# Performance work log

Hardware: AMD Instinct MI355X
Metric: run time of the kernel (lower is better)

## Reference

```python
import jax, jax.numpy as jnp
import numpy as np

B, IN_CH, SLOTS, SLOT_SIZE, READ_SLOTS = 16, 512, 10000, 256, 3


def _fa_params(key, c, scale=0.02):
    k1, k2 = jax.random.split(key)
    return (jax.random.normal(k1, (c, c), jnp.float32) * scale, jnp.zeros((c,), jnp.float32),
            jax.random.normal(k2, (c, c), jnp.float32) * scale, jnp.zeros((c,), jnp.float32))


def fast_attention(x, w1, b1, w2, b2):
    # FastAttention: x * Linear2(softmax(Linear1(x), dim=channel))
    h = jax.nn.softmax(x @ w1 + b1, axis=1)
    return x * (h @ w2 + b2)


def setup_inputs() -> dict:
    key = jax.random.key(0)
    ks = jax.random.split(key, 12)
    s = 0.02
    inp = {}
    inp["inputs"] = jax.random.normal(ks[0], (B, IN_CH), jnp.float32)
    inp["memory"] = jax.random.normal(ks[1], (B, SLOTS, SLOT_SIZE), jnp.float32)
    # read_weights branch: FastAttention(IN_CH) -> Linear(IN_CH, READ_SLOTS*SLOTS) -> tanh
    inp["fa_r_w1"], inp["fa_r_b1"], inp["fa_r_w2"], inp["fa_r_b2"] = _fa_params(ks[2], IN_CH)
    inp["W_read"] = jax.random.normal(ks[3], (IN_CH, READ_SLOTS * SLOTS), jnp.float32) * s
    inp["b_read"] = jnp.zeros((READ_SLOTS * SLOTS,), jnp.float32)
    # update_weights branch: FastAttention(IN_CH) -> Linear(IN_CH, READ_SLOTS) -> sigmoid
    inp["fa_u_w1"], inp["fa_u_b1"], inp["fa_u_w2"], inp["fa_u_b2"] = _fa_params(ks[4], IN_CH)
    inp["W_uw"] = jax.random.normal(ks[5], (IN_CH, READ_SLOTS), jnp.float32) * s
    inp["b_uw"] = jnp.zeros((READ_SLOTS,), jnp.float32)
    # update_memory branch: FastAttention(IN_CH+SLOT_SIZE) -> Linear(., SLOT_SIZE) -> relu
    inp["fa_um_w1"], inp["fa_um_b1"], inp["fa_um_w2"], inp["fa_um_b2"] = _fa_params(ks[6], IN_CH + SLOT_SIZE)
    inp["W_um"] = jax.random.normal(ks[7], (IN_CH + SLOT_SIZE, SLOT_SIZE), jnp.float32) * s
    inp["b_um"] = jnp.zeros((SLOT_SIZE,), jnp.float32)
    # apply_memory branch: FastAttention(2*SLOT_SIZE) -> Linear(., SLOT_SIZE) -> relu
    inp["fa_am_w1"], inp["fa_am_b1"], inp["fa_am_w2"], inp["fa_am_b2"] = _fa_params(ks[8], 2 * SLOT_SIZE)
    inp["W_am"] = jax.random.normal(ks[9], (2 * SLOT_SIZE, SLOT_SIZE), jnp.float32) * s
    inp["b_am"] = jnp.zeros((SLOT_SIZE,), jnp.float32)
    return inp


def reference(inputs, memory,
              fa_r_w1, fa_r_b1, fa_r_w2, fa_r_b2, W_read, b_read,
              fa_u_w1, fa_u_b1, fa_u_w2, fa_u_b2, W_uw, b_uw,
              fa_um_w1, fa_um_b1, fa_um_w2, fa_um_b2, W_um, b_um,
              fa_am_w1, fa_am_b1, fa_am_w2, fa_am_b2, W_am, b_am):
    b = inputs.shape[0]
    # read scores: [B, READ_SLOTS, SLOTS]
    read = jnp.tanh(fast_attention(inputs, fa_r_w1, fa_r_b1, fa_r_w2, fa_r_b2) @ W_read + b_read)
    read = read.reshape(b, READ_SLOTS, SLOTS)
    read_w = jnp.max(read, axis=2)                 # [B, READ_SLOTS]
    read_idx = jnp.argmax(read, axis=2)            # [B, READ_SLOTS] int
    upd_w = jax.nn.sigmoid(fast_attention(inputs, fa_u_w1, fa_u_b1, fa_u_w2, fa_u_b2) @ W_uw + b_uw)
    # gather the selected memory slots: [B, READ_SLOTS, SLOT_SIZE]
    r_all = memory[jnp.arange(b)[:, None], read_idx]
    m = jnp.zeros((b, SLOT_SIZE), inputs.dtype)
    # sequential recurrence over the (small, fixed) read_slots
    for i in range(READ_SLOTS):
        r = r_all[:, i]                            # [B, SLOT_SIZE]
        upd = jax.nn.relu(fast_attention(jnp.concatenate([r, inputs], axis=1),
                                         fa_um_w1, fa_um_b1, fa_um_w2, fa_um_b2) @ W_um + b_um)
        u = upd_w[:, i:i + 1]
        r = u * upd + (1.0 - u) * r
        m = read_w[:, i:i + 1] * jax.nn.relu(fast_attention(jnp.concatenate([r, m], axis=1),
                                                            fa_am_w1, fa_am_b1, fa_am_w2, fa_am_b2) @ W_am + b_am)
    return jnp.tanh(m)
```

## Files before the change

kernel.cpp:

```cpp
#include <hip/hip_runtime.h>
#include <cfloat>
#include <cmath>

constexpr int NTILES = 79;

enum : int {
  WS_XR    = 0,
  WS_UPDW  = 8192,
  WS_READW = 8240,
  WS_PMAX  = 8288,
  WS_PIDX  = 12080,
  WS_RNEW  = 15872,
  WS_M     = 28160,
  WS_XC    = 32256,
  WS_TPA   = 69120,
  WS_HA    = 134656,
  WS_YPA   = 151040,
  WS_TPU   = 216576,
  WS_HU    = 437760,
  WS_YPU   = 474624,
  WS_WPU   = 695808,
  WS_TPM   = 769536,
  WS_HM    = 802304,
  WS_YPM   = 810496,
  WS_WPM   = 843264,
};

__device__ __forceinline__ float wave_sum(float v) {
#pragma unroll
  for (int o = 32; o > 0; o >>= 1) v += __shfl_xor(v, o);
  return v;
}
__device__ __forceinline__ float wave_max(float v) {
#pragma unroll
  for (int o = 32; o > 0; o >>= 1) v = fmaxf(v, __shfl_xor(v, o));
  return v;
}
__device__ __forceinline__ float block_sum(float v, float* red) {
  int lane = threadIdx.x & 63, w = threadIdx.x >> 6, nw = blockDim.x >> 6;
  v = wave_sum(v);
  __syncthreads();
  if (lane == 0) red[w] = v;
  __syncthreads();
  float s = 0.f;
  for (int k = 0; k < nw; k++) s += red[k];
  return s;
}
__device__ __forceinline__ float block_max(float v, float* red) {
  int lane = threadIdx.x & 63, w = threadIdx.x >> 6, nw = blockDim.x >> 6;
  v = wave_max(v);
  __syncthreads();
  if (lane == 0) red[w] = v;
  __syncthreads();
  float s = -FLT_MAX;
  for (int k = 0; k < nw; k++) s = fmaxf(s, red[k]);
  return s;
}

__device__ __forceinline__ void mm_tile16(
    const float* __restrict__ xs,
    const float* __restrict__ W, int ldw,
    int koff, int jbase, float2& ra, float2& rb) {
  int lane = threadIdx.x & 63, w = threadIdx.x >> 6;
  const float* xa = xs + (w * 2) * 128;
  const float* xb = xa + 128;
  const float* Wp = W + (size_t)koff * ldw + jbase + lane * 2;
  float a00 = 0.f, a01 = 0.f, a10 = 0.f, a11 = 0.f;
#pragma unroll 8
  for (int k = 0; k < 128; k++) {
    float2 wv = *(const float2*)(Wp + (size_t)k * ldw);
    float xav = xa[k], xbv = xb[k];
    a00 = fmaf(xav, wv.x, a00); a01 = fmaf(xav, wv.y, a01);
    a10 = fmaf(xbv, wv.x, a10); a11 = fmaf(xbv, wv.y, a11);
  }
  ra = make_float2(a00, a01);
  rb = make_float2(a10, a11);
}
__device__ __forceinline__ void store_tile16(
    float* __restrict__ T, int ldt, int jbase, float2 ra, float2 rb) {
  int lane = threadIdx.x & 63, w = threadIdx.x >> 6;
  int r0 = w * 2, j0 = jbase + lane * 2;
  *(float2*)(T + (size_t)r0 * ldt + j0) = ra;
  *(float2*)(T + (size_t)(r0 + 1) * ldt + j0) = rb;
}

__global__ __launch_bounds__(512) void k_mm1_a(
    const float* __restrict__ x, const float* __restrict__ w1r,
    const float* __restrict__ w1u, float* __restrict__ TPA) {
  __shared__ float xs[16 * 128];
  int jt = blockIdx.x, ks = blockIdx.y, m = blockIdx.z, tid = threadIdx.x;
  for (int t = tid; t < 2048; t += 512) {
    int b = t >> 7, kk = t & 127;
    xs[t] = x[b * 512 + ks * 128 + kk];
  }
  __syncthreads();
  float2 ra, rb;
  mm_tile16(xs, m ? w1u : w1r, 512, ks * 128, jt * 128, ra, rb);
  store_tile16(TPA + (size_t)((m * 4 + ks) * 16) * 512, 512, jt * 128, ra, rb);
}

__global__ __launch_bounds__(512) void k_sm_a(
    const float* __restrict__ TPA, const float* __restrict__ b1r,
    const float* __restrict__ b1u, float* __restrict__ HA) {
  __shared__ float red[16];
  int b = blockIdx.x, m = blockIdx.y, tid = threadIdx.x;
  float t = (m ? b1u : b1r)[tid];
#pragma unroll
  for (int ks = 0; ks < 4; ks++)
    t += TPA[(size_t)((m * 4 + ks) * 16 + b) * 512 + tid];
  float mx = block_max(t, red);
  float e = expf(t - mx);
  float s = block_sum(e, red);
  HA[(size_t)(m * 16 + b) * 512 + tid] = e / s;
}

__global__ __launch_bounds__(512) void k_mm2_a(
    const float* __restrict__ HA, const float* __restrict__ w2r,
    const float* __restrict__ w2u, float* __restrict__ YPA) {
  __shared__ float xs[16 * 128];
  int jt = blockIdx.x, ks = blockIdx.y, m = blockIdx.z, tid = threadIdx.x;
  for (int t = tid; t < 2048; t += 512) {
    int b = t >> 7, kk = t & 127;
    xs[t] = HA[(size_t)(m * 16 + b) * 512 + ks * 128 + kk];
  }
  __syncthreads();
  float2 ra, rb;
  mm_tile16(xs, m ? w2u : w2r, 512, ks * 128, jt * 128, ra, rb);
  store_tile16(YPA + (size_t)((m * 4 + ks) * 16) * 512, 512, jt * 128, ra, rb);
}

__global__ __launch_bounds__(512) void k_fin_a(
    const float* __restrict__ x, const float* __restrict__ YPA,
    const float* __restrict__ b2r, const float* __restrict__ b2u,
    const float* __restrict__ Wuw, const float* __restrict__ buw,
    float* __restrict__ XR, float* __restrict__ UPDW, float* __restrict__ M) {
  __shared__ float red[16];
  int b = blockIdx.x, tid = threadIdx.x;
  float yr = b2r[tid], yu = b2u[tid];
#pragma unroll
  for (int ks = 0; ks < 4; ks++) {
    yr += YPA[(size_t)((0 + ks) * 16 + b) * 512 + tid];
    yu += YPA[(size_t)((4 + ks) * 16 + b) * 512 + tid];
  }
  float xv = x[b * 512 + tid];
  XR[b * 512 + tid] = xv * yr;
  float xu = xv * yu;
  if (tid < 256) M[b * 256 + tid] = 0.f;
  for (int i = 0; i < 3; i++) {
    float si = block_sum(xu * Wuw[tid * 3 + i], red);
    if (tid == 0) UPDW[b * 3 + i] = 1.f / (1.f + expf(-(si + buw[i])));
  }
}

__global__ __launch_bounds__(512) void k_read(
    const float* __restrict__ W, const float* __restrict__ brd,
    const float* __restrict__ xr,
    float* __restrict__ pmax, int* __restrict__ pidx) {
  __shared__ __align__(16) float xs[16 * 512];
  int tid = threadIdx.x, lane = tid & 63, w = tid >> 6;
  int i = blockIdx.y, tile = blockIdx.x;
  {
    const float4* s4 = (const float4*)xr;
    float4* d4 = (float4*)xs;
    for (int t = tid; t < 2048; t += 512) d4[t] = s4[t];
  }
  __syncthreads();
  int b0 = w * 2, b1 = b0 + 1;
  int s0 = tile * 128 + lane * 2;
  int sC = (s0 > 9998) ? 9998 : s0;
  const float* Wp = W + i * 10000 + sC;
  const float* xap = xs + b0 * 512;
  const float* xbp = xs + b1 * 512;
  float a00 = 0.f, a01 = 0.f, a10 = 0.f, a11 = 0.f;
#pragma unroll 8
  for (int c = 0; c < 512; c += 4) {
    float4 xa = *(const float4*)(xap + c);
    float4 xb = *(const float4*)(xbp + c);
    float2 w0 = *(const float2*)(Wp + (size_t)(c + 0) * 30000);
    float2 w1 = *(const float2*)(Wp + (size_t)(c + 1) * 30000);
    float2 w2 = *(const float2*)(Wp + (size_t)(c + 2) * 30000);
    float2 w3 = *(const float2*)(Wp + (size_t)(c + 3) * 30000);
    a00 = fmaf(xa.x, w0.x, a00); a01 = fmaf(xa.x, w0.y, a01);
    a10 = fmaf(xb.x, w0.x, a10); a11 = fmaf(xb.x, w0.y, a11);
    a00 = fmaf(xa.y, w1.x, a00); a01 = fmaf(xa.y, w1.y, a01);
    a10 = fmaf(xb.y, w1.x, a10); a11 = fmaf(xb.y, w1.y, a11);
    a00 = fmaf(xa.z, w2.x, a00); a01 = fmaf(xa.z, w2.y, a01);
    a10 = fmaf(xb.z, w2.x, a10); a11 = fmaf(xb.z, w2.y, a11);
    a00 = fmaf(xa.w, w3.x, a00); a01 = fmaf(xa.w, w3.y, a01);
    a10 = fmaf(xb.w, w3.x, a10); a11 = fmaf(xb.w, w3.y, a11);
  }
  float2 bb = *(const float2*)(brd + i * 10000 + sC);
  bool ok0 = (s0 < 10000), ok1 = (s0 + 1 < 10000);
  float v00 = a00 + bb.x, v01 = a01 + bb.y;
  float v10 = a10 + bb.x, v11 = a11 + bb.y;
  float bv0 = ok0 ? v00 : -FLT_MAX; int bi0 = s0;
  if (ok1 && v01 > bv0) { bv0 = v01; bi0 = s0 + 1; }
  float bv1 = ok0 ? v10 : -FLT_MAX; int bi1 = s0;
  if (ok1 && v11 > bv1) { bv1 = v11; bi1 = s0 + 1; }
#pragma unroll
  for (int o = 32; o > 0; o >>= 1) {
    float ov = __shfl_down(bv0, o); int oi = __shfl_down(bi0, o);
    if (ov > bv0) { bv0 = ov; bi0 = oi; }
    ov = __shfl_down(bv1, o); oi = __shfl_down(bi1, o);
    if (ov > bv1) { bv1 = ov; bi1 = oi; }
  }
  if (lane == 0) {
    int base = (i * 16 + b0) * NTILES + tile;
    pmax[base] = bv0; pidx[base] = bi0;
    base = (i * 16 + b1) * NTILES + tile;
    pmax[base] = bv1; pidx[base] = bi1;
  }
}

__global__ __launch_bounds__(768) void k_gather(
    const float* __restrict__ mem, const float* __restrict__ x,
    const float* __restrict__ pmax, const int* __restrict__ pidx,
    float* __restrict__ READW, float* __restrict__ XC) {
  __shared__ int sidx;
  int bi = blockIdx.x, b = bi / 3, i = bi % 3;
  int tid = threadIdx.x, lane = tid & 63;
  if (tid < 64) {
    float bv = -FLT_MAX; int bix = 0;
    const float* pm = pmax + (i * 16 + b) * NTILES;
    const int* pi = pidx + (i * 16 + b) * NTILES;
    for (int t = lane; t < NTILES; t += 64) {
      float v = pm[t]; int ix = pi[t];
      if (v > bv || (v == bv && ix < bix)) { bv = v; bix = ix; }
    }
#pragma unroll
    for (int o = 32; o > 0; o >>= 1) {
      float ov = __shfl_down(bv, o); int oi = __shfl_down(bix, o);
      if (ov > bv || (ov == bv && oi < bix)) { bv = ov; bix = oi; }
    }
    if (lane == 0) { sidx = bix; READW[bi] = tanhf(bv); }
  }
  __syncthreads();
  if (tid < 256) XC[(size_t)bi * 768 + tid] = mem[((size_t)b * 10000 + sidx) * 256 + tid];
  else           XC[(size_t)bi * 768 + tid] = x[b * 512 + (tid - 256)];
}

__global__ __launch_bounds__(512) void k_mm1_u(
    const float* __restrict__ XC, const float* __restrict__ w1um,
    float* __restrict__ TPU) {
  __shared__ float xs[16 * 128];
  int jt = blockIdx.x, ks = blockIdx.y, g = blockIdx.z, tid = threadIdx.x;
  for (int t = tid; t < 2048; t += 512) {
    int r = t >> 7, kk = t & 127;
    xs[t] = XC[(size_t)(g * 16 + r) * 768 + ks * 128 + kk];
  }
  __syncthreads();
  float2 ra, rb;
  mm_tile16(xs, w1um, 768, ks * 128, jt * 128, ra, rb);
  store_tile16(TPU + (size_t)(ks * 48 + g * 16) * 768, 768, jt * 128, ra, rb);
}

__global__ __launch_bounds__(768) void k_sm_u(
    const float* __restrict__ TPU, const float* __restrict__ b1um,
    float* __restrict__ HU) {
  __shared__ float red[16];
  int bi = blockIdx.x, tid = threadIdx.x;
  float t = b1um[tid];
#pragma unroll
  for (int ks = 0; ks < 6; ks++)
    t += TPU[(size_t)(ks * 48 + bi) * 768 + tid];
  float mx = block_max(t, red);
  float e = expf(t - mx);
  float s = block_sum(e, red);
  HU[(size_t)bi * 768 + tid] = e / s;
}

__global__ __launch_bounds__(512) void k_mm2_u(
    const float* __restrict__ HU, const float* __restrict__ w2um,
    float* __restrict__ YPU) {
  __shared__ float xs[16 * 128];
  int jt = blockIdx.x, ks = blockIdx.y, g = blockIdx.z, tid = threadIdx.x;
  for (int t = tid; t < 2048; t += 512) {
    int r = t >> 7, kk = t & 127;
    xs[t] = HU[(size_t)(g * 16 + r) * 768 + ks * 128 + kk];
  }
  __syncthreads();
  float2 ra, rb;
  mm_tile16(xs, w2um, 768, ks * 128, jt * 128, ra, rb);
  store_tile16(YPU + (size_t)(ks * 48 + g * 16) * 768, 768, jt * 128, ra, rb);
}

__global__ __launch_bounds__(512) void k_wum(
    const float* __restrict__ YPU, const float* __restrict__ XC,
    const float* __restrict__ b2um, const float* __restrict__ Wum,
    float* __restrict__ WPU) {
  __shared__ float xs[16 * 128];
  int jt = blockIdx.x, ks = blockIdx.y, g = blockIdx.z, tid = threadIdx.x;
  for (int t = tid; t < 2048; t += 512) {
    int r = t >> 7, kk = t & 127;
    int bi = g * 16 + r, k = ks * 128 + kk;
    float y = b2um[k];
#pragma unroll
    for (int k2 = 0; k2 < 6; k2++) y += YPU[(size_t)(k2 * 48 + bi) * 768 + k];
    xs[t] = XC[(size_t)bi * 768 + k] * y;
  }
  __syncthreads();
  float2 ra, rb;
  mm_tile16(xs, Wum, 256, ks * 128, jt * 128, ra, rb);
  store_tile16(WPU + (size_t)(ks * 48 + g * 16) * 256, 256, jt * 128, ra, rb);
}

__global__ __launch_bounds__(256) void k_fin_u(
    const float* __restrict__ WPU, const float* __restrict__ XC,
    const float* __restrict__ bum, const float* __restrict__ UPDW,
    float* __restrict__ RNEW) {
  int bi = blockIdx.x, tid = threadIdx.x;
  float s = bum[tid];
#pragma unroll
  for (int ks = 0; ks < 6; ks++)
    s += WPU[(size_t)(ks * 48 + bi) * 256 + tid];
  float u = UPDW[bi];
  RNEW[(size_t)bi * 256 + tid] = u * fmaxf(s, 0.f) + (1.f - u) * XC[(size_t)bi * 768 + tid];
}

__global__ __launch_bounds__(512) void k_mm1_m(
    const float* __restrict__ RNEW, const float* __restrict__ M,
    const float* __restrict__ w1am, float* __restrict__ TPM, int i) {
  __shared__ float xs[16 * 128];
  int jt = blockIdx.x, ks = blockIdx.y, tid = threadIdx.x;
  for (int t = tid; t < 2048; t += 512) {
    int b = t >> 7, kk = t & 127;
    xs[t] = (ks < 2) ? RNEW[(size_t)(b * 3 + i) * 256 + ks * 128 + kk]
                     : M[b * 256 + (ks - 2) * 128 + kk];
  }
  __syncthreads();
  float2 ra, rb;
  mm_tile16(xs, w1am, 512, ks * 128, jt * 128, ra, rb);
  store_tile16(TPM + (size_t)(ks * 16) * 512, 512, jt * 128, ra, rb);
}

__global__ __launch_bounds__(512) void k_sm_m(
    const float* __restrict__ TPM, const float* __restrict__ b1am,
    float* __restrict__ HM) {
  __shared__ float red[16];
  int b = blockIdx.x, tid = threadIdx.x;
  float t = b1am[tid];
#pragma unroll
  for (int ks = 0; ks < 4; ks++)
    t += TPM[(size_t)(ks * 16 + b) * 512 + tid];
  float mx = block_max(t, red);
  float e = expf(t - mx);
  float s = block_sum(e, red);
  HM[(size_t)b * 512 + tid] = e / s;
}

__global__ __launch_bounds__(512) void k_mm2_m(
    const float* __restrict__ HM, const float* __restrict__ w2am,
    float* __restrict__ YPM) {
  __shared__ float xs[16 * 128];
  int jt = blockIdx.x, ks = blockIdx.y, tid = threadIdx.x;
  for (int t = tid; t < 2048; t += 512) {
    int b = t >> 7, kk = t & 127;
    xs[t] = HM[(size_t)b * 512 + ks * 128 + kk];
  }
  __syncthreads();
  float2 ra, rb;
  mm_tile16(xs, w2am, 512, ks * 128, jt * 128, ra, rb);
  store_tile16(YPM + (size_t)(ks * 16) * 512, 512, jt * 128, ra, rb);
}

__global__ __launch_bounds__(512) void k_wam(
    const float* __restrict__ YPM, const float* __restrict__ RNEW,
    const float* __restrict__ M, const float* __restrict__ b2am,
    const float* __restrict__ Wam, float* __restrict__ WPM, int i) {
  __shared__ float xs[16 * 128];
  int jt = blockIdx.x, ks = blockIdx.y, tid = threadIdx.x;
  for (int t = tid; t < 2048; t += 512) {
    int b = t >> 7, kk = t & 127;
    int k = ks * 128 + kk;
    float xc = (ks < 2) ? RNEW[(size_t)(b * 3 + i) * 256 + k]
                        : M[b * 256 + k - 256];
    float y = b2am[k];
#pragma unroll
    for (int k2 = 0; k2 < 4; k2++) y += YPM[(size_t)(k2 * 16 + b) * 512 + k];
    xs[t] = xc * y;
  }
  __syncthreads();
  float2 ra, rb;
  mm_tile16(xs, Wam, 256, ks * 128, jt * 128, ra, rb);
  store_tile16(WPM + (size_t)(ks * 16) * 256, 256, jt * 128, ra, rb);
}

__global__ __launch_bounds__(256) void k_fin_m(
    const float* __restrict__ WPM, const float* __restrict__ bam,
    const float* __restrict__ READW, float* __restrict__ M,
    float* __restrict__ out, int i, int last) {
  int b = blockIdx.x, tid = threadIdx.x;
  float s = bam[tid];
#pragma unroll
  for (int ks = 0; ks < 4; ks++)
    s += WPM[(size_t)(ks * 16 + b) * 256 + tid];
  float mv = READW[b * 3 + i] * fmaxf(s, 0.f);
  M[b * 256 + tid] = mv;
  if (last) out[b * 256 + tid] = tanhf(mv);
}

extern "C" void kernel_launch(void* const* d_in, const int* in_sizes, int n_in,
                              void* d_out, int out_size, void* d_ws, size_t ws_size,
                              hipStream_t stream) {
  const float* x    = (const float*)d_in[0];
  const float* mem  = (const float*)d_in[1];
  const float* w1r  = (const float*)d_in[2];
  const float* b1r  = (const float*)d_in[3];
  const float* w2r  = (const float*)d_in[4];
  const float* b2r  = (const float*)d_in[5];
  const float* Wrd  = (const float*)d_in[6];
  const float* brd  = (const float*)d_in[7];
  const float* w1u  = (const float*)d_in[8];
  const float* b1u  = (const float*)d_in[9];
  const float* w2u  = (const float*)d_in[10];
  const float* b2u  = (const float*)d_in[11];
  const float* Wuw  = (const float*)d_in[12];
  const float* buw  = (const float*)d_in[13];
  const float* w1um = (const float*)d_in[14];
  const float* b1um = (const float*)d_in[15];
  const float* w2um = (const float*)d_in[16];
  const float* b2um = (const float*)d_in[17];
  const float* Wum  = (const float*)d_in[18];
  const float* bum  = (const float*)d_in[19];
  const float* w1am = (const float*)d_in[20];
  const float* b1am = (const float*)d_in[21];
  const float* w2am = (const float*)d_in[22];
  const float* b2am = (const float*)d_in[23];
  const float* Wam  = (const float*)d_in[24];
  const float* bam  = (const float*)d_in[25];

  float* ws   = (float*)d_ws;
  float* XR   = ws + WS_XR;
  float* UPDW = ws + WS_UPDW;
  float* RDW  = ws + WS_READW;
  float* PMAX = ws + WS_PMAX;
  int*   PIDX = (int*)(ws + WS_PIDX);
  float* RNEW = ws + WS_RNEW;
  float* M    = ws + WS_M;
  float* XC   = ws + WS_XC;
  float* TPA  = ws + WS_TPA;
  float* HA   = ws + WS_HA;
  float* YPA  = ws + WS_YPA;
  float* TPU  = ws + WS_TPU;
  float* HU   = ws + WS_HU;
  float* YPU  = ws + WS_YPU;
  float* WPU  = ws + WS_WPU;
  float* TPM  = ws + WS_TPM;
  float* HM   = ws + WS_HM;
  float* YPM  = ws + WS_YPM;
  float* WPM  = ws + WS_WPM;
  float* out  = (float*)d_out;

  k_mm1_a<<<dim3(4, 4, 2), 512, 0, stream>>>(x, w1r, w1u, TPA);
  k_sm_a <<<dim3(16, 2),   512, 0, stream>>>(TPA, b1r, b1u, HA);
  k_mm2_a<<<dim3(4, 4, 2), 512, 0, stream>>>(HA, w2r, w2u, YPA);
  k_fin_a<<<16,            512, 0, stream>>>(x, YPA, b2r, b2u, Wuw, buw,
                                             XR, UPDW, M);
  k_read  <<<dim3(NTILES, 3), 512, 0, stream>>>(Wrd, brd, XR, PMAX, PIDX);
  k_gather<<<48,              768, 0, stream>>>(mem, x, PMAX, PIDX, RDW, XC);
  k_mm1_u<<<dim3(6, 6, 3), 512, 0, stream>>>(XC, w1um, TPU);
  k_sm_u <<<48,            768, 0, stream>>>(TPU, b1um, HU);
  k_mm2_u<<<dim3(6, 6, 3), 512, 0, stream>>>(HU, w2um, YPU);
  k_wum  <<<dim3(2, 6, 3), 512, 0, stream>>>(YPU, XC, b2um, Wum, WPU);
  k_fin_u<<<48,            256, 0, stream>>>(WPU, XC, bum, UPDW, RNEW);
  for (int i = 0; i < 3; i++) {
    k_mm1_m<<<dim3(4, 4), 512, 0, stream>>>(RNEW, M, w1am, TPM, i);
    k_sm_m <<<16,         512, 0, stream>>>(TPM, b1am, HM);
    k_mm2_m<<<dim3(4, 4), 512, 0, stream>>>(HM, w2am, YPM);
    k_wam  <<<dim3(2, 4), 512, 0, stream>>>(YPM, RNEW, M, b2am, Wam, WPM, i);
    k_fin_m<<<16,         256, 0, stream>>>(WPM, bam, RDW, M, out, i, i == 2);
  }
}
```

Before: 508.1 us.

## Fuse softmax with second matmul and epilogues, dropping split-K partial kernels

Merges each FastAttention softmax with the following Linear2 matmul and the elementwise epilogue into one kernel that keeps the full softmax rows in shared memory. It also folds the update-weight sigmoid into the gather kernel, and folds the final bias/relu/mix steps into the output matmuls. This removes several launches and intermediate global buffers per stage. In exchange, each fused kernel runs the full reduction depth in very few blocks, which reduces parallelism and lengthens per-thread serial loops.

```diff
diff --git a/kernel.cpp b/kernel.cpp
--- a/kernel.cpp
+++ b/kernel.cpp
@@ -12,18 +12,13 @@
   WS_PIDX  = 12080,
   WS_RNEW  = 15872,
   WS_M     = 28160,
-  WS_XC    = 32256,
-  WS_TPA   = 69120,
-  WS_HA    = 134656,
-  WS_YPA   = 151040,
-  WS_TPU   = 216576,
-  WS_HU    = 437760,
-  WS_YPU   = 474624,
-  WS_WPU   = 695808,
-  WS_TPM   = 769536,
-  WS_HM    = 802304,
-  WS_YPM   = 810496,
-  WS_WPM   = 843264,
+  WS_XU    = 32256,
+  WS_XA    = 40448,
+  WS_TPA   = 48640,
+  WS_TPM   = 114176,
+  WS_XU2   = 146944,
+  WS_TPU   = 183808,
+  WS_XC    = 404992,
 };
 
 __device__ __forceinline__ float wave_sum(float v) {
@@ -46,21 +41,11 @@
   for (int k = 0; k < nw; k++) s += red[k];
   return s;
 }
-__device__ __forceinline__ float block_max(float v, float* red) {
-  int lane = threadIdx.x & 63, w = threadIdx.x >> 6, nw = blockDim.x >> 6;
-  v = wave_max(v);
-  __syncthreads();
-  if (lane == 0) red[w] = v;
-  __syncthreads();
-  float s = -FLT_MAX;
-  for (int k = 0; k < nw; k++) s = fmaxf(s, red[k]);
-  return s;
-}
 
 __device__ __forceinline__ void mm_tile16(
     const float* __restrict__ xs,
-    const float* __restrict__ W, int ldw,
-    int koff, int jbase, float2& ra, float2& rb) {
+    const float* __restrict__ W, int ldw, int koff, int jbase,
+    float2& ra, float2& rb) {
   int lane = threadIdx.x & 63, w = threadIdx.x >> 6;
   const float* xa = xs + (w * 2) * 128;
   const float* xb = xa + 128;
@@ -76,12 +61,50 @@
   ra = make_float2(a00, a01);
   rb = make_float2(a10, a11);
 }
+__device__ __forceinline__ void mm_rows(const float* __restrict__ xs, int ldx, int K,
+                                        const float* __restrict__ W, int ldw, int jbase,
+                                        float2& ra, float2& rb) {
+  int lane = threadIdx.x & 63, w = threadIdx.x >> 6;
+  const float* xa = xs + (w * 2) * ldx;
+  const float* xb = xa + ldx;
+  const float* Wp = W + jbase + lane * 2;
+  float a00 = 0.f, a01 = 0.f, a10 = 0.f, a11 = 0.f;
+#pragma unroll 16
+  for (int k = 0; k < K; k++) {
+    float2 wv = *(const float2*)(Wp + (size_t)k * ldw);
+    float xav = xa[k], xbv = xb[k];
+    a00 = fmaf(xav, wv.x, a00); a01 = fmaf(xav, wv.y, a01);
+    a10 = fmaf(xbv, wv.x, a10); a11 = fmaf(xbv, wv.y, a11);
+  }
+  ra = make_float2(a00, a01);
+  rb = make_float2(a10, a11);
+}
 __device__ __forceinline__ void store_tile16(
     float* __restrict__ T, int ldt, int jbase, float2 ra, float2 rb) {
   int lane = threadIdx.x & 63, w = threadIdx.x >> 6;
   int r0 = w * 2, j0 = jbase + lane * 2;
   *(float2*)(T + (size_t)r0 * ldt + j0) = ra;
   *(float2*)(T + (size_t)(r0 + 1) * ldt + j0) = rb;
+}
+
+__device__ __forceinline__ void softmax_rows(float* xs, int ncol) {
+  int lane = threadIdx.x & 63, w = threadIdx.x >> 6;
+#pragma unroll
+  for (int rr = 0; rr < 2; rr++) {
+    float* row = xs + (size_t)(w * 2 + rr) * ncol;
+    float mx = -FLT_MAX;
+    for (int j = lane; j < ncol; j += 64) mx = fmaxf(mx, row[j]);
+    mx = wave_max(mx);
+    float acc = 0.f;
+    for (int j = lane; j < ncol; j += 64) {
+      float e = expf(row[j] - mx);
+      row[j] = e;
+      acc += e;
+    }
+    acc = wave_sum(acc);
+    float inv = 1.f / acc;
+    for (int j = lane; j < ncol; j += 64) row[j] *= inv;
+  }
 }
 
 __global__ __launch_bounds__(512) void k_mm1_a(
@@ -99,57 +122,35 @@
   store_tile16(TPA + (size_t)((m * 4 + ks) * 16) * 512, 512, jt * 128, ra, rb);
 }
 
-__global__ __launch_bounds__(512) void k_sm_a(
-    const float* __restrict__ TPA, const float* __restrict__ b1r,
-    const float* __restrict__ b1u, float* __restrict__ HA) {
-  __shared__ float red[16];
-  int b = blockIdx.x, m = blockIdx.y, tid = threadIdx.x;
-  float t = (m ? b1u : b1r)[tid];
-#pragma unroll
-  for (int ks = 0; ks < 4; ks++)
-    t += TPA[(size_t)((m * 4 + ks) * 16 + b) * 512 + tid];
-  float mx = block_max(t, red);
-  float e = expf(t - mx);
-  float s = block_sum(e, red);
-  HA[(size_t)(m * 16 + b) * 512 + tid] = e / s;
-}
-
-__global__ __launch_bounds__(512) void k_mm2_a(
-    const float* __restrict__ HA, const float* __restrict__ w2r,
-    const float* __restrict__ w2u, float* __restrict__ YPA) {
-  __shared__ float xs[16 * 128];
-  int jt = blockIdx.x, ks = blockIdx.y, m = blockIdx.z, tid = threadIdx.x;
-  for (int t = tid; t < 2048; t += 512) {
-    int b = t >> 7, kk = t & 127;
-    xs[t] = HA[(size_t)(m * 16 + b) * 512 + ks * 128 + kk];
-  }
-  __syncthreads();
-  float2 ra, rb;
-  mm_tile16(xs, m ? w2u : w2r, 512, ks * 128, jt * 128, ra, rb);
-  store_tile16(YPA + (size_t)((m * 4 + ks) * 16) * 512, 512, jt * 128, ra, rb);
-}
-
-__global__ __launch_bounds__(512) void k_fin_a(
-    const float* __restrict__ x, const float* __restrict__ YPA,
+__global__ __launch_bounds__(512) void k_sm2_a(
+    const float* __restrict__ TPA, const float* __restrict__ x,
+    const float* __restrict__ b1r, const float* __restrict__ b1u,
+    const float* __restrict__ w2r, const float* __restrict__ w2u,
     const float* __restrict__ b2r, const float* __restrict__ b2u,
-    const float* __restrict__ Wuw, const float* __restrict__ buw,
-    float* __restrict__ XR, float* __restrict__ UPDW, float* __restrict__ M) {
-  __shared__ float red[16];
-  int b = blockIdx.x, tid = threadIdx.x;
-  float yr = b2r[tid], yu = b2u[tid];
-#pragma unroll
-  for (int ks = 0; ks < 4; ks++) {
-    yr += YPA[(size_t)((0 + ks) * 16 + b) * 512 + tid];
-    yu += YPA[(size_t)((4 + ks) * 16 + b) * 512 + tid];
-  }
-  float xv = x[b * 512 + tid];
-  XR[b * 512 + tid] = xv * yr;
-  float xu = xv * yu;
-  if (tid < 256) M[b * 256 + tid] = 0.f;
-  for (int i = 0; i < 3; i++) {
-    float si = block_sum(xu * Wuw[tid * 3 + i], red);
-    if (tid == 0) UPDW[b * 3 + i] = 1.f / (1.f + expf(-(si + buw[i])));
-  }
+    float* __restrict__ XR, float* __restrict__ XU) {
+  __shared__ float xs[8192];
+  int jt = blockIdx.x, m = blockIdx.y, tid = threadIdx.x;
+  int lane = tid & 63, w = tid >> 6;
+  const float* b1 = m ? b1u : b1r;
+  for (int e = tid; e < 8192; e += 512) {
+    int b = e >> 9, j = e & 511;
+    float v = b1[j];
+#pragma unroll
+    for (int ks = 0; ks < 4; ks++) v += TPA[(size_t)((m * 4 + ks) * 16 + b) * 512 + j];
+    xs[e] = v;
+  }
+  __syncthreads();
+  softmax_rows(xs, 512);
+  float2 ra, rb;
+  mm_rows(xs, 512, 512, m ? w2u : w2r, 512, jt * 128, ra, rb);
+  int r0 = w * 2, j0 = jt * 128 + lane * 2;
+  const float* b2 = m ? b2u : b2r;
+  float b20 = b2[j0], b21 = b2[j0 + 1];
+  float* dst = m ? XU : XR;
+  float2 x0 = *(const float2*)(x + r0 * 512 + j0);
+  float2 x1 = *(const float2*)(x + (r0 + 1) * 512 + j0);
+  *(float2*)(dst + r0 * 512 + j0)       = make_float2(x0.x * (ra.x + b20), x0.y * (ra.y + b21));
+  *(float2*)(dst + (r0 + 1) * 512 + j0) = make_float2(x1.x * (rb.x + b20), x1.y * (rb.y + b21));
 }
 
 __global__ __launch_bounds__(512) void k_read(
@@ -212,11 +213,14 @@
   }
 }
 
-__global__ __launch_bounds__(768) void k_gather(
+__global__ __launch_bounds__(512) void k_gather(
     const float* __restrict__ mem, const float* __restrict__ x,
     const float* __restrict__ pmax, const int* __restrict__ pidx,
-    float* __restrict__ READW, float* __restrict__ XC) {
+    const float* __restrict__ XU, const float* __restrict__ Wuw,
+    const float* __restrict__ buw,
+    float* __restrict__ RDW, float* __restrict__ UPDW, float* __restrict__ XC) {
   __shared__ int sidx;
+  __shared__ float red[16];
   int bi = blockIdx.x, b = bi / 3, i = bi % 3;
   int tid = threadIdx.x, lane = tid & 63;
   if (tid < 64) {
@@ -232,11 +236,15 @@
       float ov = __shfl_down(bv, o); int oi = __shfl_down(bix, o);
       if (ov > bv || (ov == bv && oi < bix)) { bv = ov; bix = oi; }
     }
-    if (lane == 0) { sidx = bix; READW[bi] = tanhf(bv); }
-  }
-  __syncthreads();
-  if (tid < 256) XC[(size_t)bi * 768 + tid] = mem[((size_t)b * 10000 + sidx) * 256 + tid];
-  else           XC[(size_t)bi * 768 + tid] = x[b * 512 + (tid - 256)];
+    if (lane == 0) { sidx = bix; RDW[bi] = tanhf(bv); }
+  }
+  __syncthreads();
+  for (int t = tid; t < 768; t += 512)
+    XC[(size_t)bi * 768 + t] = (t < 256)
+        ? mem[((size_t)b * 10000 + sidx) * 256 + t]
+        : x[b * 512 + (t - 256)];
+  float si = block_sum(XU[b * 512 + tid] * Wuw[tid * 3 + i], red);
+  if (tid == 0) UPDW[bi] = 1.f / (1.f + expf(-(si + buw[i])));
 }
 
 __global__ __launch_bounds__(512) void k_mm1_u(
@@ -254,67 +262,57 @@
   store_tile16(TPU + (size_t)(ks * 48 + g * 16) * 768, 768, jt * 128, ra, rb);
 }
 
-__global__ __launch_bounds__(768) void k_sm_u(
-    const float* __restrict__ TPU, const float* __restrict__ b1um,
-    float* __restrict__ HU) {
-  __shared__ float red[16];
-  int bi = blockIdx.x, tid = threadIdx.x;
-  float t = b1um[tid];
-#pragma unroll
-  for (int ks = 0; ks < 6; ks++)
-    t += TPU[(size_t)(ks * 48 + bi) * 768 + tid];
-  float mx = block_max(t, red);
-  float e = expf(t - mx);
-  float s = block_sum(e, red);
-  HU[(size_t)bi * 768 + tid] = e / s;
-}
-
-__global__ __launch_bounds__(512) void k_mm2_u(
-    const float* __restrict__ HU, const float* __restrict__ w2um,
-    float* __restrict__ YPU) {
-  __shared__ float xs[16 * 128];
-  int jt = blockIdx.x, ks = blockIdx.y, g = blockIdx.z, tid = threadIdx.x;
-  for (int t = tid; t < 2048; t += 512) {
-    int r = t >> 7, kk = t & 127;
-    xs[t] = HU[(size_t)(g * 16 + r) * 768 + ks * 128 + kk];
-  }
-  __syncthreads();
-  float2 ra, rb;
-  mm_tile16(xs, w2um, 768, ks * 128, jt * 128, ra, rb);
-  store_tile16(YPU + (size_t)(ks * 48 + g * 16) * 768, 768, jt * 128, ra, rb);
+__global__ __launch_bounds__(512) void k_sm2_u(
+    const float* __restrict__ TPU, const float* __restrict__ XC,
+    const float* __restrict__ b1um, const float* __restrict__ w2um,
+    const float* __restrict__ b2um, float* __restrict__ XU2) {
+  __shared__ float xs[12288];
+  int jt = blockIdx.x, g = blockIdx.y, tid = threadIdx.x;
+  int lane = tid & 63, w = tid >> 6;
+  for (int e = tid; e < 12288; e += 512) {
+    int r = e / 768, j = e - r * 768;
+    float v = b1um[j];
+#pragma unroll
+    for (int ks = 0; ks < 6; ks++) v += TPU[(size_t)(ks * 48 + g * 16 + r) * 768 + j];
+    xs[e] = v;
+  }
+  __syncthreads();
+  softmax_rows(xs, 768);
+  float2 ra, rb;
+  mm_rows(xs, 768, 768, w2um, 768, jt * 128, ra, rb);
+  int r0 = w * 2, j0 = jt * 128 + lane * 2, bi0 = g * 16 + r0;
+  float b0 = b2um[j0], b1v = b2um[j0 + 1];
+  float2 xc0 = *(const float2*)(XC + (size_t)bi0 * 768 + j0);
+  float2 xc1 = *(const float2*)(XC + (size_t)(bi0 + 1) * 768 + j0);
+  *(float2*)(XU2 + (size_t)bi0 * 768 + j0) =
+      make_float2(xc0.x * (ra.x + b0), xc0.y * (ra.y + b1v));
+  *(float2*)(XU2 + (size_t)(bi0 + 1) * 768 + j0) =
+      make_float2(xc1.x * (rb.x + b0), xc1.y * (rb.y + b1v));
 }
 
 __global__ __launch_bounds__(512) void k_wum(
-    const float* __restrict__ YPU, const float* __restrict__ XC,
-    const float* __restrict__ b2um, const float* __restrict__ Wum,
-    float* __restrict__ WPU) {
-  __shared__ float xs[16 * 128];
-  int jt = blockIdx.x, ks = blockIdx.y, g = blockIdx.z, tid = threadIdx.x;
-  for (int t = tid; t < 2048; t += 512) {
-    int r = t >> 7, kk = t & 127;
-    int bi = g * 16 + r, k = ks * 128 + kk;
-    float y = b2um[k];
-#pragma unroll
-    for (int k2 = 0; k2 < 6; k2++) y += YPU[(size_t)(k2 * 48 + bi) * 768 + k];
-    xs[t] = XC[(size_t)bi * 768 + k] * y;
-  }
-  __syncthreads();
-  float2 ra, rb;
-  mm_tile16(xs, Wum, 256, ks * 128, jt * 128, ra, rb);
-  store_tile16(WPU + (size_t)(ks * 48 + g * 16) * 256, 256, jt * 128, ra, rb);
-}
-
-__global__ __launch_bounds__(256) void k_fin_u(
-    const float* __restrict__ WPU, const float* __restrict__ XC,
-    const float* __restrict__ bum, const float* __restrict__ UPDW,
-    float* __restrict__ RNEW) {
-  int bi = blockIdx.x, tid = threadIdx.x;
-  float s = bum[tid];
-#pragma unroll
-  for (int ks = 0; ks < 6; ks++)
-    s += WPU[(size_t)(ks * 48 + bi) * 256 + tid];
-  float u = UPDW[bi];
-  RNEW[(size_t)bi * 256 + tid] = u * fmaxf(s, 0.f) + (1.f - u) * XC[(size_t)bi * 768 + tid];
+    const float* __restrict__ XU2, const float* __restrict__ XC,
+    const float* __restrict__ Wum, const float* __restrict__ bum,
+    const float* __restrict__ UPDW, float* __restrict__ RNEW) {
+  __shared__ float xs[12288];
+  int bid = blockIdx.x, g = bid >> 1, jt = bid & 1, tid = threadIdx.x;
+  int lane = tid & 63, w = tid >> 6;
+  const float* src = XU2 + (size_t)(g * 16) * 768;
+  for (int e = tid; e < 12288; e += 512) xs[e] = src[e];
+  __syncthreads();
+  float2 ra, rb;
+  mm_rows(xs, 768, 768, Wum, 256, jt * 128, ra, rb);
+  int r0 = w * 2, j0 = jt * 128 + lane * 2, bi0 = g * 16 + r0;
+  float bb0 = bum[j0], bb1 = bum[j0 + 1];
+  float u0 = UPDW[bi0], u1 = UPDW[bi0 + 1];
+  float2 xc0 = *(const float2*)(XC + (size_t)bi0 * 768 + j0);
+  float2 xc1 = *(const float2*)(XC + (size_t)(bi0 + 1) * 768 + j0);
+  *(float2*)(RNEW + (size_t)bi0 * 256 + j0) =
+      make_float2(u0 * fmaxf(ra.x + bb0, 0.f) + (1.f - u0) * xc0.x,
+                  u0 * fmaxf(ra.y + bb1, 0.f) + (1.f - u0) * xc0.y);
+  *(float2*)(RNEW + (size_t)(bi0 + 1) * 256 + j0) =
+      make_float2(u1 * fmaxf(rb.x + bb0, 0.f) + (1.f - u1) * xc1.x,
+                  u1 * fmaxf(rb.y + bb1, 0.f) + (1.f - u1) * xc1.y);
 }
 
 __global__ __launch_bounds__(512) void k_mm1_m(
@@ -325,7 +323,7 @@
   for (int t = tid; t < 2048; t += 512) {
     int b = t >> 7, kk = t & 127;
     xs[t] = (ks < 2) ? RNEW[(size_t)(b * 3 + i) * 256 + ks * 128 + kk]
-                     : M[b * 256 + (ks - 2) * 128 + kk];
+                     : (i == 0 ? 0.f : M[b * 256 + (ks - 2) * 128 + kk]);
   }
   __syncthreads();
   float2 ra, rb;
@@ -333,70 +331,66 @@
   store_tile16(TPM + (size_t)(ks * 16) * 512, 512, jt * 128, ra, rb);
 }
 
-__global__ __launch_bounds__(512) void k_sm_m(
-    const float* __restrict__ TPM, const float* __restrict__ b1am,
-    float* __restrict__ HM) {
-  __shared__ float red[16];
-  int b = blockIdx.x, tid = threadIdx.x;
-  float t = b1am[tid];
-#pragma unroll
-  for (int ks = 0; ks < 4; ks++)
-    t += TPM[(size_t)(ks * 16 + b) * 512 + tid];
-  float mx = block_max(t, red);
-  float e = expf(t - mx);
-  float s = block_sum(e, red);
-  HM[(size_t)b * 512 + tid] = e / s;
-}
-
-__global__ __launch_bounds__(512) void k_mm2_m(
-    const float* __restrict__ HM, const float* __restrict__ w2am,
-    float* __restrict__ YPM) {
-  __shared__ float xs[16 * 128];
-  int jt = blockIdx.x, ks = blockIdx.y, tid = threadIdx.x;
-  for (int t = tid; t < 2048; t += 512) {
-    int b = t >> 7, kk = t & 127;
-    xs[t] = HM[(size_t)b * 512 + ks * 128 + kk];
-  }
-  __syncthreads();
-  float2 ra, rb;
-  mm_tile16(xs, w2am, 512, ks * 128, jt * 128, ra, rb);
-  store_tile16(YPM + (size_t)(ks * 16) * 512, 512, jt * 128, ra, rb);
+__global__ __launch_bounds__(512) void k_sm2_m(
+    const float* __restrict__ TPM, const float* __restrict__ RNEW,
+    const float* __restrict__ M, const float* __restrict__ b1am,
+    const float* __restrict__ w2am, const float* __restrict__ b2am,
+    float* __restrict__ XA, int i) {
+  __shared__ float xs[8192];
+  int jt = blockIdx.x, tid = threadIdx.x;
+  int lane = tid & 63, w = tid >> 6;
+  for (int e = tid; e < 8192; e += 512) {
+    int b = e >> 9, j = e & 511;
+    float v = b1am[j];
+#pragma unroll
+    for (int ks = 0; ks < 4; ks++) v += TPM[(size_t)(ks * 16 + b) * 512 + j];
+    xs[e] = v;
+  }
+  __syncthreads();
+  softmax_rows(xs, 512);
+  float2 ra, rb;
+  mm_rows(xs, 512, 512, w2am, 512, jt * 128, ra, rb);
+  int r0 = w * 2, j0 = jt * 128 + lane * 2;
+  float b0 = b2am[j0], b1v = b2am[j0 + 1];
+  float2 c0, c1;
+  if (j0 < 256) {
+    c0 = *(const float2*)(RNEW + (size_t)(r0 * 3 + i) * 256 + j0);
+    c1 = *(const float2*)(RNEW + (size_t)((r0 + 1) * 3 + i) * 256 + j0);
+  } else if (i == 0) {
+    c0 = make_float2(0.f, 0.f);
+    c1 = make_float2(0.f, 0.f);
+  } else {
+    c0 = *(const float2*)(M + r0 * 256 + (j0 - 256));
+    c1 = *(const float2*)(M + (r0 + 1) * 256 + (j0 - 256));
+  }
+  *(float2*)(XA + r0 * 512 + j0) =
+      make_float2(c0.x * (ra.x + b0), c0.y * (ra.y + b1v));
+  *(float2*)(XA + (r0 + 1) * 512 + j0) =
+      make_float2(c1.x * (rb.x + b0), c1.y * (rb.y + b1v));
 }
 
 __global__ __launch_bounds__(512) void k_wam(
-    const float* __restrict__ YPM, const float* __restrict__ RNEW,
-    const float* __restrict__ M, const float* __restrict__ b2am,
-    const float* __restrict__ Wam, float* __restrict__ WPM, int i) {
-  __shared__ float xs[16 * 128];
-  int jt = blockIdx.x, ks = blockIdx.y, tid = threadIdx.x;
-  for (int t = tid; t < 2048; t += 512) {
-    int b = t >> 7, kk = t & 127;
-    int k = ks * 128 + kk;
-    float xc = (ks < 2) ? RNEW[(size_t)(b * 3 + i) * 256 + k]
-                        : M[b * 256 + k - 256];
-    float y = b2am[k];
-#pragma unroll
-    for (int k2 = 0; k2 < 4; k2++) y += YPM[(size_t)(k2 * 16 + b) * 512 + k];
-    xs[t] = xc * y;
-  }
-  __syncthreads();
-  float2 ra, rb;
-  mm_tile16(xs, Wam, 256, ks * 128, jt * 128, ra, rb);
-  store_tile16(WPM + (size_t)(ks * 16) * 256, 256, jt * 128, ra, rb);
-}
-
-__global__ __launch_bounds__(256) void k_fin_m(
-    const float* __restrict__ WPM, const float* __restrict__ bam,
-    const float* __restrict__ READW, float* __restrict__ M,
-    float* __restrict__ out, int i, int last) {
-  int b = blockIdx.x, tid = threadIdx.x;
-  float s = bam[tid];
-#pragma unroll
-  for (int ks = 0; ks < 4; ks++)
-    s += WPM[(size_t)(ks * 16 + b) * 256 + tid];
-  float mv = READW[b * 3 + i] * fmaxf(s, 0.f);
-  M[b * 256 + tid] = mv;
-  if (last) out[b * 256 + tid] = tanhf(mv);
+    const float* __restrict__ XA, const float* __restrict__ Wam,
+    const float* __restrict__ bam, const float* __restrict__ RDW,
+    float* __restrict__ M, float* __restrict__ out, int i, int last) {
+  __shared__ float xs[8192];
+  int jt = blockIdx.x, tid = threadIdx.x;
+  int lane = tid & 63, w = tid >> 6;
+  for (int e = tid; e < 8192; e += 512) xs[e] = XA[e];
+  __syncthreads();
+  float2 ra, rb;
+  mm_rows(xs, 512, 512, Wam, 256, jt * 128, ra, rb);
+  int r0 = w * 2, j0 = jt * 128 + lane * 2;
+  float bb0 = bam[j0], bb1 = bam[j0 + 1];
+  float u0 = RDW[r0 * 3 + i], u1 = RDW[(r0 + 1) * 3 + i];
+  float m00 = u0 * fmaxf(ra.x + bb0, 0.f), m01 = u0 * fmaxf(ra.y + bb1, 0.f);
+  float m10 = u1 * fmaxf(rb.x + bb0, 0.f), m11 = u1 * fmaxf(rb.y + bb1, 0.f);
+  *(float2*)(M + r0 * 256 + j0) = make_float2(m00, m01);
+  *(float2*)(M + (r0 + 1) * 256 + j0) = make_float2(m10, m11);
+  if (last) {
+    *(float2*)(out + r0 * 256 + j0) = make_float2(tanhf(m00), tanhf(m01));
+    *(float2*)(out + (r0 + 1) * 256 + j0) = make_float2(tanhf(m10), tanhf(m11));
+  }
 }
 
 extern "C" void kernel_launch(void* const* d_in, const int* in_sizes, int n_in,
@@ -437,37 +431,27 @@
   int*   PIDX = (int*)(ws + WS_PIDX);
   float* RNEW = ws + WS_RNEW;
   float* M    = ws + WS_M;
+  float* XU   = ws + WS_XU;
+  float* XA   = ws + WS_XA;
+  float* TPA  = ws + WS_TPA;
+  float* TPM  = ws + WS_TPM;
+  float* XU2  = ws + WS_XU2;
+  float* TPU  = ws + WS_TPU;
   float* XC   = ws + WS_XC;
-  float* TPA  = ws + WS_TPA;
-  float* HA   = ws + WS_HA;
-  float* YPA  = ws + WS_YPA;
-  float* TPU  = ws + WS_TPU;
-  float* HU   = ws + WS_HU;
-  float* YPU  = ws + WS_YPU;
-  float* WPU  = ws + WS_WPU;
-  float* TPM  = ws + WS_TPM;
-  float* HM   = ws + WS_HM;
-  float* YPM  = ws + WS_YPM;
-  float* WPM  = ws + WS_WPM;
   float* out  = (float*)d_out;
 
   k_mm1_a<<<dim3(4, 4, 2), 512, 0, stream>>>(x, w1r, w1u, TPA);
-  k_sm_a <<<dim3(16, 2),   512, 0, stream>>>(TPA, b1r, b1u, HA);
-  k_mm2_a<<<dim3(4, 4, 2), 512, 0, stream>>>(HA, w2r, w2u, YPA);
-  k_fin_a<<<16,            512, 0, stream>>>(x, YPA, b2r, b2u, Wuw, buw,
-                                             XR, UPDW, M);
+  k_sm2_a<<<dim3(4, 2),    512, 0, stream>>>(TPA, x, b1r, b1u, w2r, w2u,
+                                             b2r, b2u, XR, XU);
   k_read  <<<dim3(NTILES, 3), 512, 0, stream>>>(Wrd, brd, XR, PMAX, PIDX);
-  k_gather<<<48,              768, 0, stream>>>(mem, x, PMAX, PIDX, RDW, XC);
+  k_gather<<<48,              512, 0, stream>>>(mem, x, PMAX, PIDX, XU,
+                                                Wuw, buw, RDW, UPDW, XC);
   k_mm1_u<<<dim3(6, 6, 3), 512, 0, stream>>>(XC, w1um, TPU);
-  k_sm_u <<<48,            768, 0, stream>>>(TPU, b1um, HU);
-  k_mm2_u<<<dim3(6, 6, 3), 512, 0, stream>>>(HU, w2um, YPU);
-  k_wum  <<<dim3(2, 6, 3), 512, 0, stream>>>(YPU, XC, b2um, Wum, WPU);
-  k_fin_u<<<48,            256, 0, stream>>>(WPU, XC, bum, UPDW, RNEW);
+  k_sm2_u<<<dim3(6, 3),    512, 0, stream>>>(TPU, XC, b1um, w2um, b2um, XU2);
+  k_wum  <<<6,             512, 0, stream>>>(XU2, XC, Wum, bum, UPDW, RNEW);
   for (int i = 0; i < 3; i++) {
     k_mm1_m<<<dim3(4, 4), 512, 0, stream>>>(RNEW, M, w1am, TPM, i);
-    k_sm_m <<<16,         512, 0, stream>>>(TPM, b1am, HM);
-    k_mm2_m<<<dim3(4, 4), 512, 0, stream>>>(HM, w2am, YPM);
-    k_wam  <<<dim3(2, 4), 512, 0, stream>>>(YPM, RNEW, M, b2am, Wam, WPM, i);
-    k_fin_m<<<16,         256, 0, stream>>>(WPM, bam, RDW, M, out, i, i == 2);
-  }
-}
+    k_sm2_m<<<4,          512, 0, stream>>>(TPM, RNEW, M, b1am, w2am, b2am, XA, i);
+    k_wam  <<<2,          512, 0, stream>>>(XA, Wam, bam, RDW, M, out, i, i == 2);
+  }
+}
```

After: 731.9 us. 1.44x slower.
